# Kernel tuning notes

Measured on AMD Instinct MI355X. Metric: run time of the kernel, lower is better.

Reference implementation:

```python
import jax, jax.numpy as jnp
import numpy as np

SAMPLE_RATE = 48000
MIX = 0.5
DELAYS_SEC = [0.0297, 0.0371, 0.0411, 0.0437, 0.0533, 0.0617, 0.0731, 0.0797]
DELAYS = [int(d * SAMPLE_RATE) for d in DELAYS_SEC]  # integer sample delays
N = len(DELAYS)
T = 8388608  # ~175 s of mono audio at 48 kHz


def setup_inputs() -> dict:
    key = jax.random.key(0)
    k1, k2, k3 = jax.random.split(key, 3)
    input_sig = jax.random.normal(k1, (1, T), dtype=jnp.float32)
    feedback_gain = jax.random.uniform(k2, (N,), dtype=jnp.float32)
    # orthogonal mix matrix via QR of a random Gaussian, as in the module's __init__
    rm = np.asarray(jax.random.normal(k3, (N, N), dtype=jnp.float32))
    q, _ = np.linalg.qr(rm)
    orthogonal_matrix = jnp.asarray(q, dtype=jnp.float32)
    return {"input_sig": input_sig, "feedback_gain": feedback_gain,
            "orthogonal_matrix": orthogonal_matrix}


def reference(input_sig, feedback_gain, orthogonal_matrix):
    x = input_sig[0]  # [T]
    # Delay buffers start at zero, so each delay line's output is the input
    # shifted right by `d` samples and zero-padded at the front.
    shifted = jnp.stack(
        [jnp.concatenate([jnp.zeros((d,), x.dtype), x[: x.shape[0] - d]]) for d in DELAYS],
        axis=0)  # [N, T]
    # sum_j (Q @ (g[:,None]*shifted))[j] == (ones @ Q) * g  dotted with shifted rows
    combined = (jnp.sum(orthogonal_matrix, axis=0) * feedback_gain)  # [N]
    wet = jnp.einsum('n,nt->t', combined, shifted)[None, :]  # [1, T]
    out = wet * MIX + input_sig * (1.0 - MIX)
    out = out / jnp.max(jnp.abs(out))
    return out
```

## Files before the change

kernel.cpp:

```cpp
#include <hip/hip_runtime.h>

#define T_LEN 8388608
#define CHUNK 4096
#define HALO  3840
#define LDSF  (HALO + CHUNK)
#define NBLK  (T_LEN / CHUNK)

#define D0 1425
#define D1 1780
#define D2 1972
#define D3 2097
#define D4 2558
#define D5 2961
#define D6 3508
#define D7 3825

typedef float floatx4 __attribute__((ext_vector_type(4)));

__device__ __forceinline__ int swz(int b) {
    return (b & 7) * (NBLK / 8) + (b >> 3);
}

template <int D>
__device__ __forceinline__ void tap4(const float* __restrict__ p, float v[4]) {
    constexpr int r = (4 - (D & 3)) & 3;
    const float* q = p - D - r;
    float4 w0 = *(const float4*)q;
    if constexpr (r == 0) {
        v[0] = w0.x; v[1] = w0.y; v[2] = w0.z; v[3] = w0.w;
    } else {
        float4 w1 = *(const float4*)(q + 4);
        float w[8] = {w0.x, w0.y, w0.z, w0.w, w1.x, w1.y, w1.z, w1.w};
#pragma unroll
        for (int k = 0; k < 4; ++k) v[k] = w[r + k];
    }
}

__device__ __forceinline__ float4 quad_fir(const float* __restrict__ p,
                                           const float* __restrict__ c) {
    float4 dry = *(const float4*)(p);
    float t0v[4], t1v[4], t2v[4], t3v[4], t4v[4], t5v[4], t6v[4], t7v[4];
    tap4<D0>(p, t0v);
    tap4<D1>(p, t1v);
    tap4<D2>(p, t2v);
    tap4<D3>(p, t3v);
    tap4<D4>(p, t4v);
    tap4<D5>(p, t5v);
    tap4<D6>(p, t6v);
    tap4<D7>(p, t7v);

    float4 o;
#pragma unroll
    for (int k = 0; k < 4; ++k) {
        float wet = 0.f;
        wet = fmaf(c[0], t0v[k], wet);
        wet = fmaf(c[1], t1v[k], wet);
        wet = fmaf(c[2], t2v[k], wet);
        wet = fmaf(c[3], t3v[k], wet);
        wet = fmaf(c[4], t4v[k], wet);
        wet = fmaf(c[5], t5v[k], wet);
        wet = fmaf(c[6], t6v[k], wet);
        wet = fmaf(c[7], t7v[k], wet);
        (&o.x)[k] = fmaf(0.5f, wet, 0.5f * (&dry.x)[k]);
    }
    return o;
}

__device__ __forceinline__ void stage(const float* __restrict__ x, float* smem,
                                      int blk, int tid) {
    const long gs = (long)blk * CHUNK - HALO;
    for (int v4 = tid; v4 < LDSF / 4; v4 += 256) {
        long ga = gs + (long)v4 * 4;
        float4 val = make_float4(0.f, 0.f, 0.f, 0.f);
        if (ga >= 0) val = *(const float4*)(x + ga);
        *(float4*)(smem + v4 * 4) = val;
    }
}

__device__ __forceinline__ void load_coeffs(const float* __restrict__ g,
                                            const float* __restrict__ Q,
                                            float* csh, int tid) {
    if (tid < 8) {
        float s = 0.f;
#pragma unroll
        for (int j = 0; j < 8; ++j) s += Q[j * 8 + tid];
        csh[tid] = s * g[tid];
    }
}

__global__ __launch_bounds__(256) void fdn_wet(
    const float* __restrict__ x, const float* __restrict__ g,
    const float* __restrict__ Q, float* __restrict__ slots,
    float* __restrict__ out) {
    __shared__ __align__(16) float smem[LDSF];
    __shared__ float csh[8];
    __shared__ float wmax[4];

    const int tid = threadIdx.x;
    const int blk = swz(blockIdx.x);

    load_coeffs(g, Q, csh, tid);
    stage(x, smem, blk, tid);
    __syncthreads();

    float c[8];
#pragma unroll
    for (int n = 0; n < 8; ++n) c[n] = csh[n];

    const int base = blk * CHUNK;
    float m = 0.f;
#pragma unroll
    for (int i = 0; i < CHUNK / 1024; ++i) {
        const int j = i * 1024 + tid * 4;
        float4 o = quad_fir(smem + HALO + j, c);
        m = fmaxf(m, fmaxf(fmaxf(fabsf(o.x), fabsf(o.y)),
                           fmaxf(fabsf(o.z), fabsf(o.w))));
        *(float4*)(out + base + j) = o;
    }

#pragma unroll
    for (int off = 32; off > 0; off >>= 1) m = fmaxf(m, __shfl_down(m, off, 64));
    if ((tid & 63) == 0) wmax[tid >> 6] = m;
    __syncthreads();
    if (tid == 0)
        slots[blk] = fmaxf(fmaxf(wmax[0], wmax[1]), fmaxf(wmax[2], wmax[3]));
}

__global__ __launch_bounds__(256) void fdn_scale(
    const float* __restrict__ slots, float* __restrict__ out) {
    __shared__ float wmax[4];

    const int tid = threadIdx.x;
    const int blk = swz(blockIdx.x);

    float4 s0 = *(const float4*)(slots + tid * 8);
    float4 s1 = *(const float4*)(slots + tid * 8 + 4);
    float m = fmaxf(fmaxf(fmaxf(s0.x, s0.y), fmaxf(s0.z, s0.w)),
                    fmaxf(fmaxf(s1.x, s1.y), fmaxf(s1.z, s1.w)));
#pragma unroll
    for (int off = 32; off > 0; off >>= 1) m = fmaxf(m, __shfl_down(m, off, 64));
    if ((tid & 63) == 0) wmax[tid >> 6] = m;
    __syncthreads();
    const float inv = 1.0f / fmaxf(fmaxf(wmax[0], wmax[1]),
                                   fmaxf(wmax[2], wmax[3]));

    const int base = blk * CHUNK;
#pragma unroll
    for (int i = 0; i < CHUNK / 1024; ++i) {
        const int j = i * 1024 + tid * 4;
        float4 v = *(const float4*)(out + base + j);
        floatx4 ov;
        ov.x = v.x * inv; ov.y = v.y * inv;
        ov.z = v.z * inv; ov.w = v.w * inv;
        __builtin_nontemporal_store(ov, (floatx4*)(out + base + j));
    }
}

extern "C" void kernel_launch(void* const* d_in, const int* in_sizes, int n_in,
                              void* d_out, int out_size, void* d_ws, size_t ws_size,
                              hipStream_t stream) {
    const float* x = (const float*)d_in[0];
    const float* g = (const float*)d_in[1];
    const float* Q = (const float*)d_in[2];
    float* out = (float*)d_out;
    float* slots = (float*)d_ws;

    fdn_wet  <<<dim3(NBLK), dim3(256), 0, stream>>>(x, g, Q, slots, out);
    fdn_scale<<<dim3(NBLK), dim3(256), 0, stream>>>(slots, out);
}
```

Baseline: 111.2 us.

## Fuse wet and scale kernels into one persistent kernel with grid barrier

Replaces the two-kernel wet/scale pipeline with a single persistent kernel of 512 blocks, each processing four chunks. The blocks combine the global max with an atomicMax on float bits, which is valid only because the values are non-negative, then spin on an atomic counter before rescaling their own chunks. This removes a kernel launch boundary and the separate slot reduction, and the block's own freshly written output may still sit in cache when it is rescaled. In exchange it relies on all 512 blocks being co-resident to avoid deadlock, and it adds a memset launch.

```diff
diff --git a/kernel.cpp b/kernel.cpp
--- a/kernel.cpp
+++ b/kernel.cpp
@@ -1,10 +1,12 @@
 #include <hip/hip_runtime.h>
 
-#define T_LEN 8388608
-#define CHUNK 4096
-#define HALO  3840
-#define LDSF  (HALO + CHUNK)
-#define NBLK  (T_LEN / CHUNK)
+#define T_LEN  8388608
+#define CHUNK  4096
+#define HALO   3840
+#define LDSF   (HALO + CHUNK)
+#define NCHUNK (T_LEN / CHUNK)
+#define NBLOCKS 512
+#define CPB    (NCHUNK / NBLOCKS)
 
 #define D0 1425
 #define D1 1780
@@ -16,10 +18,6 @@
 #define D7 3825
 
 typedef float floatx4 __attribute__((ext_vector_type(4)));
-
-__device__ __forceinline__ int swz(int b) {
-    return (b & 7) * (NBLK / 8) + (b >> 3);
-}
 
 template <int D>
 __device__ __forceinline__ void tap4(const float* __restrict__ p, float v[4]) {
@@ -67,8 +65,8 @@
 }
 
 __device__ __forceinline__ void stage(const float* __restrict__ x, float* smem,
-                                      int blk, int tid) {
-    const long gs = (long)blk * CHUNK - HALO;
+                                      int ch, int tid) {
+    const long gs = (long)ch * CHUNK - HALO;
     for (int v4 = tid; v4 < LDSF / 4; v4 += 256) {
         long ga = gs + (long)v4 * 4;
         float4 val = make_float4(0.f, 0.f, 0.f, 0.f);
@@ -88,71 +86,75 @@
     }
 }
 
-__global__ __launch_bounds__(256) void fdn_wet(
+__global__ __launch_bounds__(256) void fdn_fused(
     const float* __restrict__ x, const float* __restrict__ g,
-    const float* __restrict__ Q, float* __restrict__ slots,
+    const float* __restrict__ Q, unsigned int* __restrict__ gsync,
     float* __restrict__ out) {
     __shared__ __align__(16) float smem[LDSF];
     __shared__ float csh[8];
     __shared__ float wmax[4];
+    __shared__ float sinv;
 
     const int tid = threadIdx.x;
-    const int blk = swz(blockIdx.x);
+    const int p   = blockIdx.x;
+    const int c0 = (p & 7) * (NCHUNK / 8) + (p >> 3) * CPB;
 
     load_coeffs(g, Q, csh, tid);
-    stage(x, smem, blk, tid);
-    __syncthreads();
 
     float c[8];
-#pragma unroll
-    for (int n = 0; n < 8; ++n) c[n] = csh[n];
-
-    const int base = blk * CHUNK;
     float m = 0.f;
 #pragma unroll
-    for (int i = 0; i < CHUNK / 1024; ++i) {
-        const int j = i * 1024 + tid * 4;
-        float4 o = quad_fir(smem + HALO + j, c);
-        m = fmaxf(m, fmaxf(fmaxf(fabsf(o.x), fabsf(o.y)),
-                           fmaxf(fabsf(o.z), fabsf(o.w))));
-        *(float4*)(out + base + j) = o;
+    for (int cc = 0; cc < CPB; ++cc) {
+        stage(x, smem, c0 + cc, tid);
+        __syncthreads();
+        if (cc == 0) {
+#pragma unroll
+            for (int n = 0; n < 8; ++n) c[n] = csh[n];
+        }
+        const int base = (c0 + cc) * CHUNK;
+#pragma unroll
+        for (int i = 0; i < CHUNK / 1024; ++i) {
+            const int j = i * 1024 + tid * 4;
+            float4 o = quad_fir(smem + HALO + j, c);
+            m = fmaxf(m, fmaxf(fmaxf(fabsf(o.x), fabsf(o.y)),
+                               fmaxf(fabsf(o.z), fabsf(o.w))));
+            *(float4*)(out + base + j) = o;
+        }
+        __syncthreads();
     }
 
 #pragma unroll
     for (int off = 32; off > 0; off >>= 1) m = fmaxf(m, __shfl_down(m, off, 64));
     if ((tid & 63) == 0) wmax[tid >> 6] = m;
     __syncthreads();
-    if (tid == 0)
-        slots[blk] = fmaxf(fmaxf(wmax[0], wmax[1]), fmaxf(wmax[2], wmax[3]));
-}
 
-__global__ __launch_bounds__(256) void fdn_scale(
-    const float* __restrict__ slots, float* __restrict__ out) {
-    __shared__ float wmax[4];
+    if (tid == 0) {
+        float bm = fmaxf(fmaxf(wmax[0], wmax[1]), fmaxf(wmax[2], wmax[3]));
+        atomicMax(gsync, __float_as_uint(bm));
+        __threadfence();
+        __hip_atomic_fetch_add(gsync + 1, 1u, __ATOMIC_RELEASE,
+                               __HIP_MEMORY_SCOPE_AGENT);
+        while (__hip_atomic_load(gsync + 1, __ATOMIC_ACQUIRE,
+                                 __HIP_MEMORY_SCOPE_AGENT) < (unsigned)NBLOCKS)
+            __builtin_amdgcn_s_sleep(8);
+        sinv = 1.0f / __uint_as_float(__hip_atomic_load(
+                         gsync, __ATOMIC_RELAXED, __HIP_MEMORY_SCOPE_AGENT));
+    }
+    __syncthreads();
+    const float inv = sinv;
 
-    const int tid = threadIdx.x;
-    const int blk = swz(blockIdx.x);
-
-    float4 s0 = *(const float4*)(slots + tid * 8);
-    float4 s1 = *(const float4*)(slots + tid * 8 + 4);
-    float m = fmaxf(fmaxf(fmaxf(s0.x, s0.y), fmaxf(s0.z, s0.w)),
-                    fmaxf(fmaxf(s1.x, s1.y), fmaxf(s1.z, s1.w)));
 #pragma unroll
-    for (int off = 32; off > 0; off >>= 1) m = fmaxf(m, __shfl_down(m, off, 64));
-    if ((tid & 63) == 0) wmax[tid >> 6] = m;
-    __syncthreads();
-    const float inv = 1.0f / fmaxf(fmaxf(wmax[0], wmax[1]),
-                                   fmaxf(wmax[2], wmax[3]));
-
-    const int base = blk * CHUNK;
+    for (int cc = 0; cc < CPB; ++cc) {
+        const int base = (c0 + cc) * CHUNK;
 #pragma unroll
-    for (int i = 0; i < CHUNK / 1024; ++i) {
-        const int j = i * 1024 + tid * 4;
-        float4 v = *(const float4*)(out + base + j);
-        floatx4 ov;
-        ov.x = v.x * inv; ov.y = v.y * inv;
-        ov.z = v.z * inv; ov.w = v.w * inv;
-        __builtin_nontemporal_store(ov, (floatx4*)(out + base + j));
+        for (int i = 0; i < CHUNK / 1024; ++i) {
+            const int j = i * 1024 + tid * 4;
+            float4 v = *(const float4*)(out + base + j);
+            floatx4 ov;
+            ov.x = v.x * inv; ov.y = v.y * inv;
+            ov.z = v.z * inv; ov.w = v.w * inv;
+            __builtin_nontemporal_store(ov, (floatx4*)(out + base + j));
+        }
     }
 }
 
@@ -163,8 +165,8 @@
     const float* g = (const float*)d_in[1];
     const float* Q = (const float*)d_in[2];
     float* out = (float*)d_out;
-    float* slots = (float*)d_ws;
+    unsigned int* gsync = (unsigned int*)d_ws;
 
-    fdn_wet  <<<dim3(NBLK), dim3(256), 0, stream>>>(x, g, Q, slots, out);
-    fdn_scale<<<dim3(NBLK), dim3(256), 0, stream>>>(slots, out);
+    hipMemsetAsync(d_ws, 0, 2 * sizeof(unsigned int), stream);
+    fdn_fused<<<dim3(NBLOCKS), dim3(256), 0, stream>>>(x, g, Q, gsync, out);
 }
```

Measured after the change: 184.1 us. 1.66x slower.

## Recompute FIR in second pass instead of storing and rereading unnormalized output

Applied to the files above, without the earlier changes.

The first kernel now computes only the per-block max of the wet/dry mix and no longer writes the intermediate output. The second kernel restages the input, recomputes the 8-tap FIR and writes the normalized result directly. This removes one full write and one full read of the output buffer in exchange for re-reading the input and doing the FIR arithmetic twice.

```diff
diff --git a/kernel.cpp b/kernel.cpp
--- a/kernel.cpp
+++ b/kernel.cpp
@@ -88,10 +88,9 @@
     }
 }
 
-__global__ __launch_bounds__(256) void fdn_wet(
+__global__ __launch_bounds__(256) void fdn_max(
     const float* __restrict__ x, const float* __restrict__ g,
-    const float* __restrict__ Q, float* __restrict__ slots,
-    float* __restrict__ out) {
+    const float* __restrict__ Q, float* __restrict__ slots) {
     __shared__ __align__(16) float smem[LDSF];
     __shared__ float csh[8];
     __shared__ float wmax[4];
@@ -107,15 +106,13 @@
 #pragma unroll
     for (int n = 0; n < 8; ++n) c[n] = csh[n];
 
-    const int base = blk * CHUNK;
     float m = 0.f;
 #pragma unroll
     for (int i = 0; i < CHUNK / 1024; ++i) {
-        const int j = i * 1024 + tid * 4;
-        float4 o = quad_fir(smem + HALO + j, c);
+        const float* p = smem + HALO + i * 1024 + tid * 4;
+        float4 o = quad_fir(p, c);
         m = fmaxf(m, fmaxf(fmaxf(fabsf(o.x), fabsf(o.y)),
                            fmaxf(fabsf(o.z), fabsf(o.w))));
-        *(float4*)(out + base + j) = o;
     }
 
 #pragma unroll
@@ -126,32 +123,46 @@
         slots[blk] = fmaxf(fmaxf(wmax[0], wmax[1]), fmaxf(wmax[2], wmax[3]));
 }
 
-__global__ __launch_bounds__(256) void fdn_scale(
-    const float* __restrict__ slots, float* __restrict__ out) {
+__global__ __launch_bounds__(256) void fdn_write(
+    const float* __restrict__ x, const float* __restrict__ g,
+    const float* __restrict__ Q, const float* __restrict__ slots,
+    float* __restrict__ out) {
+    __shared__ __align__(16) float smem[LDSF];
+    __shared__ float csh[8];
     __shared__ float wmax[4];
 
     const int tid = threadIdx.x;
     const int blk = swz(blockIdx.x);
 
+    load_coeffs(g, Q, csh, tid);
+
     float4 s0 = *(const float4*)(slots + tid * 8);
     float4 s1 = *(const float4*)(slots + tid * 8 + 4);
+
+    stage(x, smem, blk, tid);
+
     float m = fmaxf(fmaxf(fmaxf(s0.x, s0.y), fmaxf(s0.z, s0.w)),
                     fmaxf(fmaxf(s1.x, s1.y), fmaxf(s1.z, s1.w)));
 #pragma unroll
     for (int off = 32; off > 0; off >>= 1) m = fmaxf(m, __shfl_down(m, off, 64));
     if ((tid & 63) == 0) wmax[tid >> 6] = m;
     __syncthreads();
+
     const float inv = 1.0f / fmaxf(fmaxf(wmax[0], wmax[1]),
                                    fmaxf(wmax[2], wmax[3]));
+    float c[8];
+#pragma unroll
+    for (int n = 0; n < 8; ++n) c[n] = csh[n];
 
     const int base = blk * CHUNK;
 #pragma unroll
     for (int i = 0; i < CHUNK / 1024; ++i) {
         const int j = i * 1024 + tid * 4;
-        float4 v = *(const float4*)(out + base + j);
+        const float* p = smem + HALO + j;
+        float4 o = quad_fir(p, c);
         floatx4 ov;
-        ov.x = v.x * inv; ov.y = v.y * inv;
-        ov.z = v.z * inv; ov.w = v.w * inv;
+        ov.x = o.x * inv; ov.y = o.y * inv;
+        ov.z = o.z * inv; ov.w = o.w * inv;
         __builtin_nontemporal_store(ov, (floatx4*)(out + base + j));
     }
 }
@@ -165,6 +176,6 @@
     float* out = (float*)d_out;
     float* slots = (float*)d_ws;
 
-    fdn_wet  <<<dim3(NBLK), dim3(256), 0, stream>>>(x, g, Q, slots, out);
-    fdn_scale<<<dim3(NBLK), dim3(256), 0, stream>>>(slots, out);
+    fdn_max  <<<dim3(NBLK), dim3(256), 0, stream>>>(x, g, Q, slots);
+    fdn_write<<<dim3(NBLK), dim3(256), 0, stream>>>(x, g, Q, slots, out);
 }
```

New measurement: 109.0 us. About the same (-1.9%).
